# Optimization experiments

Measured on AMD Instinct MI355X. Metric: run time of the kernel, lower is better.

## Reference

```python
import jax, jax.numpy as jnp
import numpy as np
from jax import lax

N_BOXES = 6000
IOU_THR = 0.5
CONF_THR = 0.6


def setup_inputs() -> dict:
    key = jax.random.key(0)
    k1, k2, k3 = jax.random.split(key, 3)
    # valid xyxy boxes: top-left in [0,1000), width/height in [1,101)
    xy = jax.random.uniform(k1, (N_BOXES, 2), dtype=jnp.float32) * 1000.0
    wh = jax.random.uniform(k2, (N_BOXES, 2), dtype=jnp.float32) * 100.0 + 1.0
    boxes = jnp.concatenate([xy, xy + wh], axis=-1)  # [N,4] x1,y1,x2,y2
    scores = jax.random.uniform(k3, (N_BOXES,), dtype=jnp.float32)
    return {"boxes": boxes, "scores": scores}


def _pairwise_iou(b):
    # b: [N,4] xyxy. Returns [N,N] IoU, coordinates handled separately to
    # avoid materializing [N,N,2] intermediates.
    x1, y1, x2, y2 = b[:, 0], b[:, 1], b[:, 2], b[:, 3]
    area = (x2 - x1) * (y2 - y1)  # [N]
    iw = jnp.clip(jnp.minimum(x2[:, None], x2[None, :]) - jnp.maximum(x1[:, None], x1[None, :]), 0.0)
    ih = jnp.clip(jnp.minimum(y2[:, None], y2[None, :]) - jnp.maximum(y1[:, None], y1[None, :]), 0.0)
    inter = iw * ih  # [N,N]
    return inter / (area[:, None] + area[None, :] - inter)


def reference(boxes, scores):
    """torchvision-style NMS (suppress IoU > 0.5) then confidence filter (>= 0.6).
    Returns masked scores [N]: score where the box survives both stages, else 0.
    (Fixed-shape mask form of the original index outputs, for jit compatibility.)
    """
    n = scores.shape[0]
    order = jnp.argsort(-scores)  # descending by confidence
    iou = _pairwise_iou(boxes[order])  # [N,N] in sorted order
    idx = jnp.arange(n)

    def body(suppressed, i):
        keep_i = jnp.logical_not(suppressed[i])
        # a kept box suppresses all lower-scoring boxes with IoU > threshold
        supp_new = keep_i & (iou[i] > IOU_THR) & (idx > i)
        return suppressed | supp_new, keep_i

    _, keep_sorted = lax.scan(body, jnp.zeros((n,), dtype=bool), idx)
    keep = jnp.zeros((n,), dtype=bool).at[order].set(keep_sorted)
    final = keep & (scores >= CONF_THR)
    return jnp.where(final, scores, 0.0)
```

## Files before the change

kernel.cpp:

```cpp
#include <hip/hip_runtime.h>
#include <stdint.h>

#define N_BOXES 6000
#define NT 94
#define NTP 96
#define NROWS (NTP * 64)
#define CAP 16
#define IOU_THR 0.5f
#define CONF_THR 0.6f

typedef unsigned long long u64;
typedef unsigned int u32;
typedef unsigned short u16;

__device__ __forceinline__ u64 rdlane64(u64 v, int l) {
    unsigned lo = (unsigned)__builtin_amdgcn_readlane((int)(unsigned)v, l);
    unsigned hi = (unsigned)__builtin_amdgcn_readlane((int)(unsigned)(v >> 32), l);
    return ((u64)hi << 32) | lo;
}

__global__ void __launch_bounds__(1024) k_sort(const float* __restrict__ scores,
                                               const float4* __restrict__ boxes,
                                               int* __restrict__ sidx,
                                               float4* __restrict__ sboxes,
                                               u32* __restrict__ lists_w,
                                               int* __restrict__ cnt) {
    __shared__ u64 kt[N_BOXES];
    __shared__ int part[1024];
    const int tid = threadIdx.x;
    const int gtid = blockIdx.x * 1024 + tid;
    for (int j = gtid; j < NROWS * CAP / 2; j += NT * 1024) lists_w[j] = 0xFFFFFFFFu;
    for (int j = gtid; j < NROWS; j += NT * 1024) cnt[j] = 0;

    for (int j = tid; j < N_BOXES; j += 1024) {
        unsigned inv = ~__float_as_uint(scores[j]);
        kt[j] = ((u64)inv << 32) | (unsigned)j;
    }
    __syncthreads();
    const int il = tid & 63;
    const int i = blockIdx.x * 64 + il;
    const int j0 = (tid >> 6) * 375;
    u64 mykey = (i < N_BOXES) ? kt[i] : 0ull;
    int cntr = 0;
#pragma unroll 5
    for (int jj = 0; jj < 375; ++jj)
        cntr += (kt[j0 + jj] < mykey) ? 1 : 0;
    part[tid] = cntr;
    __syncthreads();
    if (tid < 64 && i < N_BOXES) {
        int r = 0;
#pragma unroll
        for (int s = 0; s < 16; ++s) r += part[il + 64 * s];
        sidx[r] = i;
        sboxes[r] = boxes[i];
    }
}

__global__ void k_mask(const float4* __restrict__ sboxes,
                       u16* __restrict__ lists, int* __restrict__ cnt,
                       u64* __restrict__ diagw) {
    int ct = blockIdx.x, rt = blockIdx.y;
    if (ct < rt) return;
    int lane = threadIdx.x;
    __shared__ float4 rb[64];
    int row0 = rt * 64;
    int rows = min(64, N_BOXES - row0);
    if (lane < rows) rb[lane] = sboxes[row0 + lane];
    __syncthreads();
    int j = ct * 64 + lane;
    bool jvalid = (j < N_BOXES);
    float4 cb = make_float4(0.f, 0.f, 1.f, 1.f);
    if (jvalid) cb = sboxes[j];
    float carea = (cb.z - cb.x) * (cb.w - cb.y);
    bool isdiag = (ct == rt);
    for (int i = 0; i < rows; ++i) {
        float4 rbx = rb[i];
        float rarea = (rbx.z - rbx.x) * (rbx.w - rbx.y);
        float iw = fmaxf(fminf(rbx.z, cb.z) - fmaxf(rbx.x, cb.x), 0.f);
        float ih = fmaxf(fminf(rbx.w, cb.w) - fmaxf(rbx.y, cb.y), 0.f);
        float inter = iw * ih;
        float iou = inter / ((rarea + carea) - inter);
        int row = row0 + i;
        bool pred = jvalid && (j > row) && (iou > IOU_THR);
        if (isdiag) {
            u64 bal = __ballot(pred);
            if (lane == (i & 63)) diagw[row] = bal;
        } else if (pred) {
            int slot = atomicAdd(&cnt[row], 1);
            if (slot < CAP) lists[row * CAP + slot] = (u16)j;
        }
    }
}

__global__ void __launch_bounds__(64) k_scan(const u16* __restrict__ lists,
                                             const u64* __restrict__ diagw,
                                             u64* __restrict__ keep) {
    __shared__ u64 removed[NTP];
    const int lane = threadIdx.x;
    removed[lane] = 0;
    if (lane < NTP - 64) removed[64 + lane] = 0;

    u64 A0[3], A1[3], A2[3], A3[3], D[3];
#pragma unroll
    for (int b = 0; b < 3; ++b) {
        const u64* lp = (const u64*)&lists[(b * 64 + lane) * CAP];
        A0[b] = lp[0]; A1[b] = lp[1]; A2[b] = lp[2]; A3[b] = lp[3];
        D[b] = diagw[b * 64 + lane];
    }

#define SCAT(W)                                                                 \
    if (W != ~0ull) {                                                           \
        u16 e0 = (u16)(W), e1 = (u16)(W >> 16),                                 \
            e2 = (u16)(W >> 32), e3 = (u16)(W >> 48);                           \
        if (e0 != 0xFFFFu) atomicOr(&removed[e0 >> 6], 1ull << (e0 & 63));      \
        if (e1 != 0xFFFFu) atomicOr(&removed[e1 >> 6], 1ull << (e1 & 63));      \
        if (e2 != 0xFFFFu) atomicOr(&removed[e2 >> 6], 1ull << (e2 & 63));      \
        if (e3 != 0xFFFFu) atomicOr(&removed[e3 >> 6], 1ull << (e3 & 63));      \
    }

#define STEP(T, B)                                                              \
    {                                                                           \
        const u64 d = D[B];                                                     \
        const u64 nz = __ballot(d != 0ull);            \
        const int rem = N_BOXES - (T) * 64;                                     \
        const u64 valid = (rem >= 64) ? ~0ull                                   \
                        : ((rem <= 0) ? 0ull : ((1ull << rem) - 1ull));         \
        u64 c = valid & ~removed[(T)];           \
        u64 kw = 0;                                                             \
        while (c) {                                                             \
            u64 blockers = c & nz;                                              \
            if (!blockers) { kw |= c; break; }              \
            int g = (int)__builtin_ctzll(blockers);                             \
            u64 below = c & ((1ull << g) - 1ull);                               \
            kw |= below | (1ull << g);                                          \
            u64 df = rdlane64(d, g);                         \
            c &= ~(df | below | (1ull << g));                                   \
        }                                                                       \
        if (lane == 0) keep[(T)] = kw;                     \
        if ((kw >> lane) & 1ull) {                                              \
            u64 w0 = A0[B], w1 = A1[B], w2 = A2[B], w3 = A3[B];                 \
            SCAT(w0) SCAT(w1) SCAT(w2) SCAT(w3)                                 \
        }                                                                       \
        const int tn = ((T) + 3 < NTP) ? ((T) + 3) : ((T) + 3 - NTP);           \
        const u64* lp = (const u64*)&lists[(tn * 64 + lane) * CAP];             \
        A0[B] = lp[0]; A1[B] = lp[1]; A2[B] = lp[2]; A3[B] = lp[3];             \
        D[B] = diagw[tn * 64 + lane];                                           \
    }

    for (int t = 0; t < NTP; t += 3) {
        STEP(t,     0)
        STEP(t + 1, 1)
        STEP(t + 2, 2)
    }
#undef STEP
#undef SCAT
}

__global__ void __launch_bounds__(256) k_out(const int* __restrict__ sidx,
                                             const float* __restrict__ scores,
                                             const u64* __restrict__ keep,
                                             float* __restrict__ out) {
    int p = blockIdx.x * 256 + threadIdx.x;
    if (p < N_BOXES) {
        int orig = sidx[p];
        float s = scores[orig];
        bool k = (keep[p >> 6] >> (p & 63)) & 1ull;
        out[orig] = (k && (s >= CONF_THR)) ? s : 0.0f;
    }
}

extern "C" void kernel_launch(void* const* d_in, const int* in_sizes, int n_in,
                              void* d_out, int out_size, void* d_ws, size_t ws_size,
                              hipStream_t stream) {
    const float* boxes  = (const float*)d_in[0];
    const float* scores = (const float*)d_in[1];
    float* out = (float*)d_out;

    char* ws = (char*)d_ws;
    u16*    lists  = (u16*)(ws);
    int*    cnt    = (int*)(ws + 196608);
    u64*    diagw  = (u64*)(ws + 221184);
    int*    sidx   = (int*)(ws + 270336);
    float4* sboxes = (float4*)(ws + 294336);
    u64*    keep   = (u64*)(ws + 390336);

    k_sort<<<dim3(NT), dim3(1024), 0, stream>>>(scores, (const float4*)boxes, sidx,
                                                sboxes, (u32*)lists, cnt);
    k_mask<<<dim3(NT, NT), dim3(64), 0, stream>>>((const float4*)sboxes, lists, cnt, diagw);
    k_scan<<<dim3(1), dim3(64), 0, stream>>>(lists, diagw, keep);
    k_out <<<dim3(24), dim3(256), 0, stream>>>(sidx, scores, keep, out);
}
```

Before: 134.9 us.

## Replace per-row suppression lists with global edge list and in-LDS CSR build

The mask kernel now appends every suppressing pair (row, col) to a single global edge array through one atomic counter, using 256-thread blocks instead of 64-thread tiles. The scan kernel then runs with 1024 threads, builds a CSR adjacency in shared memory via a histogram, a prefix scan and a scatter, and performs the greedy NMS sweep on one wavefront, deriving diagonal masks from the CSR. This drops the per-row list initialisation and the fixed per-row capacity, but adds heavy contention on one global atomic, puts the CSR build on the serial critical path, and silently truncates past ECAP edges.

Measured after the change: 151.1 us. 12.0% more time.

```diff
diff --git a/kernel.cpp b/kernel.cpp
--- a/kernel.cpp
+++ b/kernel.cpp
@@ -3,9 +3,8 @@
 
 #define N_BOXES 6000
 #define NT 94
-#define NTP 96
-#define NROWS (NTP * 64)
-#define CAP 16
+#define NROWS 6144
+#define ECAP 16384
 #define IOU_THR 0.5f
 #define CONF_THR 0.6f
 
@@ -23,14 +22,11 @@
                                                const float4* __restrict__ boxes,
                                                int* __restrict__ sidx,
                                                float4* __restrict__ sboxes,
-                                               u32* __restrict__ lists_w,
-                                               int* __restrict__ cnt) {
+                                               int* __restrict__ ecnt) {
     __shared__ u64 kt[N_BOXES];
     __shared__ int part[1024];
     const int tid = threadIdx.x;
-    const int gtid = blockIdx.x * 1024 + tid;
-    for (int j = gtid; j < NROWS * CAP / 2; j += NT * 1024) lists_w[j] = 0xFFFFFFFFu;
-    for (int j = gtid; j < NROWS; j += NT * 1024) cnt[j] = 0;
+    if (blockIdx.x == 0 && tid == 0) *ecnt = 0;
 
     for (int j = tid; j < N_BOXES; j += 1024) {
         unsigned inv = ~__float_as_uint(scores[j]);
@@ -56,23 +52,22 @@
     }
 }
 
-__global__ void k_mask(const float4* __restrict__ sboxes,
-                       u16* __restrict__ lists, int* __restrict__ cnt,
-                       u64* __restrict__ diagw) {
-    int ct = blockIdx.x, rt = blockIdx.y;
-    if (ct < rt) return;
-    int lane = threadIdx.x;
+__global__ void __launch_bounds__(256) k_mask(const float4* __restrict__ sboxes,
+                                              u32* __restrict__ edges,
+                                              int* __restrict__ ecnt) {
+    const int rt = blockIdx.y;
+    const int row0 = rt * 64;
+    if (blockIdx.x * 256 + 255 < row0) return;
+    const int tid = threadIdx.x;
     __shared__ float4 rb[64];
-    int row0 = rt * 64;
-    int rows = min(64, N_BOXES - row0);
-    if (lane < rows) rb[lane] = sboxes[row0 + lane];
-    __syncthreads();
-    int j = ct * 64 + lane;
-    bool jvalid = (j < N_BOXES);
+    const int rows = min(64, N_BOXES - row0);
+    if (tid < rows) rb[tid] = sboxes[row0 + tid];
+    __syncthreads();
+    const int j = blockIdx.x * 256 + tid;
+    const bool jvalid = (j < N_BOXES);
     float4 cb = make_float4(0.f, 0.f, 1.f, 1.f);
     if (jvalid) cb = sboxes[j];
-    float carea = (cb.z - cb.x) * (cb.w - cb.y);
-    bool isdiag = (ct == rt);
+    const float carea = (cb.z - cb.x) * (cb.w - cb.y);
     for (int i = 0; i < rows; ++i) {
         float4 rbx = rb[i];
         float rarea = (rbx.z - rbx.x) * (rbx.w - rbx.y);
@@ -81,79 +76,104 @@
         float inter = iw * ih;
         float iou = inter / ((rarea + carea) - inter);
         int row = row0 + i;
-        bool pred = jvalid && (j > row) && (iou > IOU_THR);
-        if (isdiag) {
-            u64 bal = __ballot(pred);
-            if (lane == (i & 63)) diagw[row] = bal;
-        } else if (pred) {
-            int slot = atomicAdd(&cnt[row], 1);
-            if (slot < CAP) lists[row * CAP + slot] = (u16)j;
+        if (jvalid && (j > row) && (iou > IOU_THR)) {
+            int e = atomicAdd(ecnt, 1);
+            if (e < ECAP) edges[e] = ((u32)row << 16) | (u32)j;
         }
     }
 }
 
-__global__ void __launch_bounds__(64) k_scan(const u16* __restrict__ lists,
-                                             const u64* __restrict__ diagw,
-                                             u64* __restrict__ keep) {
-    __shared__ u64 removed[NTP];
-    const int lane = threadIdx.x;
-    removed[lane] = 0;
-    if (lane < NTP - 64) removed[64 + lane] = 0;
-
-    u64 A0[3], A1[3], A2[3], A3[3], D[3];
+__global__ void __launch_bounds__(1024) k_scan(const u32* __restrict__ edges,
+                                               const int* __restrict__ ecnt,
+                                               u64* __restrict__ keep) {
+    __shared__ u32 rowptr[NROWS];
+    __shared__ u16 csr[ECAP];
+    __shared__ u64 removed[NT];
+    __shared__ u32 aux[16];
+    const int tid  = threadIdx.x;
+    const int lane = tid & 63;
+    const int wv   = tid >> 6;
+
+    {
+        int b = tid * 6;
 #pragma unroll
-    for (int b = 0; b < 3; ++b) {
-        const u64* lp = (const u64*)&lists[(b * 64 + lane) * CAP];
-        A0[b] = lp[0]; A1[b] = lp[1]; A2[b] = lp[2]; A3[b] = lp[3];
-        D[b] = diagw[b * 64 + lane];
-    }
-
-#define SCAT(W)                                                                 \
-    if (W != ~0ull) {                                                           \
-        u16 e0 = (u16)(W), e1 = (u16)(W >> 16),                                 \
-            e2 = (u16)(W >> 32), e3 = (u16)(W >> 48);                           \
-        if (e0 != 0xFFFFu) atomicOr(&removed[e0 >> 6], 1ull << (e0 & 63));      \
-        if (e1 != 0xFFFFu) atomicOr(&removed[e1 >> 6], 1ull << (e1 & 63));      \
-        if (e2 != 0xFFFFu) atomicOr(&removed[e2 >> 6], 1ull << (e2 & 63));      \
-        if (e3 != 0xFFFFu) atomicOr(&removed[e3 >> 6], 1ull << (e3 & 63));      \
-    }
-
-#define STEP(T, B)                                                              \
-    {                                                                           \
-        const u64 d = D[B];                                                     \
-        const u64 nz = __ballot(d != 0ull);            \
-        const int rem = N_BOXES - (T) * 64;                                     \
-        const u64 valid = (rem >= 64) ? ~0ull                                   \
-                        : ((rem <= 0) ? 0ull : ((1ull << rem) - 1ull));         \
-        u64 c = valid & ~removed[(T)];           \
-        u64 kw = 0;                                                             \
-        while (c) {                                                             \
-            u64 blockers = c & nz;                                              \
-            if (!blockers) { kw |= c; break; }              \
-            int g = (int)__builtin_ctzll(blockers);                             \
-            u64 below = c & ((1ull << g) - 1ull);                               \
-            kw |= below | (1ull << g);                                          \
-            u64 df = rdlane64(d, g);                         \
-            c &= ~(df | below | (1ull << g));                                   \
-        }                                                                       \
-        if (lane == 0) keep[(T)] = kw;                     \
-        if ((kw >> lane) & 1ull) {                                              \
-            u64 w0 = A0[B], w1 = A1[B], w2 = A2[B], w3 = A3[B];                 \
-            SCAT(w0) SCAT(w1) SCAT(w2) SCAT(w3)                                 \
-        }                                                                       \
-        const int tn = ((T) + 3 < NTP) ? ((T) + 3) : ((T) + 3 - NTP);           \
-        const u64* lp = (const u64*)&lists[(tn * 64 + lane) * CAP];             \
-        A0[B] = lp[0]; A1[B] = lp[1]; A2[B] = lp[2]; A3[B] = lp[3];             \
-        D[B] = diagw[tn * 64 + lane];                                           \
-    }
-
-    for (int t = 0; t < NTP; t += 3) {
-        STEP(t,     0)
-        STEP(t + 1, 1)
-        STEP(t + 2, 2)
-    }
-#undef STEP
-#undef SCAT
+        for (int k = 0; k < 6; ++k) rowptr[b + k] = 0;
+        if (tid < NT) removed[tid] = 0;
+    }
+    __syncthreads();
+
+    int ne = *ecnt;
+    if (ne > ECAP) ne = ECAP;
+
+    for (int i = tid; i < ne; i += 1024)
+        atomicAdd(&rowptr[edges[i] >> 16], 1u);
+    __syncthreads();
+
+    {
+        int b = tid * 6;
+        u32 c0 = rowptr[b], c1 = rowptr[b + 1], c2 = rowptr[b + 2],
+            c3 = rowptr[b + 3], c4 = rowptr[b + 4], c5 = rowptr[b + 5];
+        u32 s = c0 + c1 + c2 + c3 + c4 + c5;
+        u32 inc = s;
+        for (int off = 1; off < 64; off <<= 1) {
+            u32 v = __shfl_up(inc, off);
+            if (lane >= off) inc += v;
+        }
+        if (lane == 63) aux[wv] = inc;
+        __syncthreads();
+        u32 woff = 0;
+        for (int w = 0; w < wv; ++w) woff += aux[w];
+        u32 run = woff + inc - s;
+        rowptr[b] = run; run += c0;
+        rowptr[b + 1] = run; run += c1;
+        rowptr[b + 2] = run; run += c2;
+        rowptr[b + 3] = run; run += c3;
+        rowptr[b + 4] = run; run += c4;
+        rowptr[b + 5] = run;
+    }
+    __syncthreads();
+
+    for (int i = tid; i < ne; i += 1024) {
+        u32 e = edges[i];
+        u32 slot = atomicAdd(&rowptr[e >> 16], 1u);
+        csr[slot] = (u16)(e & 0xFFFFu);
+    }
+    __syncthreads();
+
+    if (wv == 0) {
+        for (int t = 0; t < NT; ++t) {
+            const int r = t * 64 + lane;
+            const u32 end = rowptr[r];
+            const u32 beg = (r == 0) ? 0u : rowptr[r - 1];
+            const int lim = (t + 1) * 64;
+            u64 d = 0;
+            for (u32 k = beg; k < end; ++k) {
+                int col = csr[k];
+                if (col < lim) d |= 1ull << (col & 63);
+            }
+            const u64 nz = __ballot(d != 0ull);
+            const int rem = N_BOXES - t * 64;
+            const u64 valid = (rem >= 64) ? ~0ull : ((1ull << rem) - 1ull);
+            u64 c = valid & ~removed[t];
+            u64 kw = 0;
+            while (c) {
+                u64 blockers = c & nz;
+                if (!blockers) { kw |= c; break; }
+                int g = (int)__builtin_ctzll(blockers);
+                u64 below = c & ((1ull << g) - 1ull);
+                kw |= below | (1ull << g);
+                u64 df = rdlane64(d, g);
+                c &= ~(df | below | (1ull << g));
+            }
+            if (lane == 0) keep[t] = kw;
+            if ((kw >> lane) & 1ull) {
+                for (u32 k = beg; k < end; ++k) {
+                    int col = csr[k];
+                    atomicOr(&removed[col >> 6], 1ull << (col & 63));
+                }
+            }
+        }
+    }
 }
 
 __global__ void __launch_bounds__(256) k_out(const int* __restrict__ sidx,
@@ -177,16 +197,15 @@
     float* out = (float*)d_out;
 
     char* ws = (char*)d_ws;
-    u16*    lists  = (u16*)(ws);
-    int*    cnt    = (int*)(ws + 196608);
-    u64*    diagw  = (u64*)(ws + 221184);
-    int*    sidx   = (int*)(ws + 270336);
-    float4* sboxes = (float4*)(ws + 294336);
-    u64*    keep   = (u64*)(ws + 390336);
-
-    k_sort<<<dim3(NT), dim3(1024), 0, stream>>>(scores, (const float4*)boxes, sidx,
-                                                sboxes, (u32*)lists, cnt);
-    k_mask<<<dim3(NT, NT), dim3(64), 0, stream>>>((const float4*)sboxes, lists, cnt, diagw);
-    k_scan<<<dim3(1), dim3(64), 0, stream>>>(lists, diagw, keep);
+    u32*    edges  = (u32*)(ws);
+    int*    ecnt   = (int*)(ws + 65536);
+    int*    sidx   = (int*)(ws + 65552);
+    float4* sboxes = (float4*)(ws + 89552);
+    u64*    keep   = (u64*)(ws + 185552);
+
+    k_sort<<<dim3(NT), dim3(1024), 0, stream>>>(scores, (const float4*)boxes,
+                                                sidx, sboxes, ecnt);
+    k_mask<<<dim3(24, NT), dim3(256), 0, stream>>>((const float4*)sboxes, edges, ecnt);
+    k_scan<<<dim3(1), dim3(1024), 0, stream>>>(edges, ecnt, keep);
     k_out <<<dim3(24), dim3(256), 0, stream>>>(sidx, scores, keep, out);
 }
```
